# Kernel optimization log

Hardware: AMD Instinct MI355X
Metric: run time of the kernel (lower is better)

Reference implementation:

```python
import jax, jax.numpy as jnp
import numpy as np

B, C, H, W = 8, 512, 64, 64
S = 64
STD = 0.001  # torch init.normal_(weight, std=0.001)


def setup_inputs() -> dict:
    key = jax.random.key(0)
    ks = jax.random.split(key, 7)
    return {
        "queries": jax.random.normal(ks[0], (B, C, H, W), dtype=jnp.float32),
        "k": jax.random.normal(ks[1], (B, C, H, W), dtype=jnp.float32),
        "v": jax.random.normal(ks[2], (B, C, H, W), dtype=jnp.float32),
        "Wq": jax.random.normal(ks[3], (S, C), dtype=jnp.float32) * STD,
        "Wk": jax.random.normal(ks[4], (S, C), dtype=jnp.float32) * STD,
        "Wv": jax.random.normal(ks[5], (S, C), dtype=jnp.float32) * STD,
        "Wl": jax.random.normal(ks[6], (C, S), dtype=jnp.float32) * STD,
    }


def _branch(A, Bp, Cp, Wl):
    # A,Bp,Cp: [h,w,b,S] projected tensors
    m = jnp.einsum('hwbs,hwbt->hwst', A, Bp)          # [h,w,S,S]
    m = jax.nn.softmax(m, axis=1)                      # softmax over w (dim=1, as in torch)
    o = jnp.einsum('hwst,hwbt->hwsb', m, Cp)           # [h,w,S,b]
    o = o / jnp.sum(o, axis=2, keepdims=True)          # normalize over S
    o = jnp.einsum('hwsb,cs->hwbc', o, Wl)             # transpose + Linear(S->C)
    return jnp.transpose(o, (2, 3, 0, 1))              # [b,c,h,w]


def reference(queries, k, v, Wq, Wk, Wv, Wl):
    q = jnp.transpose(queries, (2, 3, 0, 1))  # [h,w,b,c]
    kk = jnp.transpose(k, (2, 3, 0, 1))
    vv = jnp.transpose(v, (2, 3, 0, 1))
    aq = jnp.einsum('hwbc,sc->hwbs', q, Wq)   # [h,w,b,S]
    ak = jnp.einsum('hwbc,sc->hwbs', kk, Wk)
    av = jnp.einsum('hwbc,sc->hwbs', vv, Wv)
    out_q = _branch(aq, ak, av, Wl)
    out_k = _branch(ak, av, aq, Wl)
    out_v = _branch(av, aq, ak, Wl)
    return jnp.concatenate((out_q, out_k, out_v), axis=0)  # [3b,c,h,w]
```

## Files before the change

### kernel.cpp

```cpp
#include <hip/hip_runtime.h>
#include <hip/hip_bf16.h>

#define HW 4096
#define CCH 512
#define SDIM 64
#define BDIM 8

typedef __attribute__((ext_vector_type(8))) short short8;
typedef __attribute__((ext_vector_type(4))) float f32x4;

static __device__ __forceinline__ ushort f2bf(float f) {
  __hip_bfloat16 h = __float2bfloat16(f);
  return *reinterpret_cast<ushort*>(&h);
}
static __device__ __forceinline__ float bf2f(ushort u) {
  union { unsigned int u32; float f; } c;
  c.u32 = ((unsigned int)u) << 16;
  return c.f;
}
static __device__ __forceinline__ ushort trunc_bf(float f, float* rem) {
  union { float f; unsigned int u; } a; a.f = f;
  union { float f; unsigned int u; } h; h.u = a.u & 0xFFFF0000u;
  *rem = f - h.f;
  return (ushort)(a.u >> 16);
}
static __device__ __forceinline__ ushort rne_bf(float f) {
  union { float f; unsigned int u; } a; a.f = f;
  return (ushort)((a.u + 0x8000u) >> 16);
}
static __device__ __forceinline__ void gll16(const float* g, float* lds_base) {
  __builtin_amdgcn_global_load_lds(
      (const __attribute__((address_space(1))) unsigned int*)g,
      (__attribute__((address_space(3))) unsigned int*)lds_base, 16, 0, 0);
}

__global__ __launch_bounds__(256) void prep_kernel(const float* __restrict__ Wq,
                                                   const float* __restrict__ Wk,
                                                   const float* __restrict__ Wv,
                                                   const float* __restrict__ Wl,
                                                   ushort* __restrict__ whi,
                                                   ushort* __restrict__ wmid,
                                                   ushort* __restrict__ wlo,
                                                   ushort* __restrict__ wlhi,
                                                   ushort* __restrict__ wllo) {
  const int idx = blockIdx.x * 1024 + threadIdx.x * 4;
  if (blockIdx.y == 3) {
    float4 f = *reinterpret_cast<const float4*>(&Wl[idx]);
    ushort4 h, l;
    float r;
    h.x = trunc_bf(f.x, &r); l.x = rne_bf(r);
    h.y = trunc_bf(f.y, &r); l.y = rne_bf(r);
    h.z = trunc_bf(f.z, &r); l.z = rne_bf(r);
    h.w = trunc_bf(f.w, &r); l.w = rne_bf(r);
    *reinterpret_cast<ushort4*>(&wlhi[idx]) = h;
    *reinterpret_cast<ushort4*>(&wllo[idx]) = l;
    return;
  }
  const float* W = blockIdx.y == 0 ? Wq : (blockIdx.y == 1 ? Wk : Wv);
  float4 f = *reinterpret_cast<const float4*>(&W[idx]);
  ushort4 h, m, l;
  float r, r2;
  h.x = f2bf(f.x); r = f.x - bf2f(h.x); m.x = f2bf(r); r2 = r - bf2f(m.x); l.x = f2bf(r2);
  h.y = f2bf(f.y); r = f.y - bf2f(h.y); m.y = f2bf(r); r2 = r - bf2f(m.y); l.y = f2bf(r2);
  h.z = f2bf(f.z); r = f.z - bf2f(h.z); m.z = f2bf(r); r2 = r - bf2f(m.z); l.z = f2bf(r2);
  h.w = f2bf(f.w); r = f.w - bf2f(h.w); m.w = f2bf(r); r2 = r - bf2f(m.w); l.w = f2bf(r2);
  const size_t o = (size_t)blockIdx.y * (SDIM * CCH) + idx;
  *reinterpret_cast<ushort4*>(&whi[o])  = h;
  *reinterpret_cast<ushort4*>(&wmid[o]) = m;
  *reinterpret_cast<ushort4*>(&wlo[o])  = l;
}

__global__ __launch_bounds__(256) void proj_mfma_kernel(const float* __restrict__ q,
                                                        const float* __restrict__ k,
                                                        const float* __restrict__ v,
                                                        const ushort* __restrict__ whi,
                                                        const ushort* __restrict__ wmid,
                                                        const ushort* __restrict__ wlo,
                                                        float* __restrict__ ap) {
  __shared__ float Xs[2 * 32 * 128];
  const int mt = blockIdx.x;
  const int b = blockIdx.y;
  const int br = blockIdx.z;
  const float* x = br == 0 ? q : (br == 1 ? k : v);
  const ushort* wh = whi + (size_t)br * SDIM * CCH;
  const ushort* wm = wmid + (size_t)br * SDIM * CCH;
  const ushort* wl = wlo + (size_t)br * SDIM * CCH;
  float* apo = ap + (size_t)br * HW * 512;
  const int hw0 = mt * 128;
  const int tid = threadIdx.x;
  const int l = tid & 63;
  const int wid = tid >> 6;
  const int wstrip = wid * 32;
  const int row16 = l & 15;
  const int kgrp = l >> 4;
  const float* xcol = x + (size_t)b * CCH * HW + hw0;
  const int rbase = 8 * wid;
  const int rsub = l >> 5;
  const int hws = (l & 31) * 4;

  f32x4 acc_hi[2][4] = {};
  f32x4 acc_co[2][4] = {};

#pragma unroll
  for (int j = 0; j < 4; ++j) {
    const int r = rbase + 2 * j + rsub;
    gll16(xcol + (size_t)r * HW + hws, &Xs[(rbase + 2 * j) * 128]);
  }

  for (int ci = 0; ci < 16; ++ci) {
    short8 bh[4], bm[4], bl[4];
#pragma unroll
    for (int nf = 0; nf < 4; ++nf) {
      const size_t off = (size_t)(nf * 16 + row16) * CCH + ci * 32 + kgrp * 8;
      bh[nf] = *reinterpret_cast<const short8*>(&wh[off]);
      bm[nf] = *reinterpret_cast<const short8*>(&wm[off]);
      bl[nf] = *reinterpret_cast<const short8*>(&wl[off]);
    }
    __builtin_amdgcn_sched_barrier(0);
    if (ci < 15) {
      float* dst = &Xs[((ci + 1) & 1) * 4096];
#pragma unroll
      for (int j = 0; j < 4; ++j) {
        const int r = rbase + 2 * j + rsub;
        gll16(xcol + (size_t)((ci + 1) * 32 + r) * HW + hws, dst + (rbase + 2 * j) * 128);
      }
      __builtin_amdgcn_sched_barrier(0);
      asm volatile("s_waitcnt vmcnt(4)" ::: "memory");
    } else {
      asm volatile("s_waitcnt vmcnt(0)" ::: "memory");
    }
    __builtin_amdgcn_sched_barrier(0);
    __builtin_amdgcn_s_barrier();
    __builtin_amdgcn_sched_barrier(0);

    const float* lw = &Xs[(ci & 1) * 4096];
#pragma unroll
    for (int mf = 0; mf < 2; ++mf) {
      const int rowA = wstrip + mf * 16 + row16;
      short8 ah, am, al;
      {
        ushort th[8], tm[8], tl[8];
#pragma unroll
        for (int i = 0; i < 8; ++i) {
          const float f = lw[(kgrp * 8 + i) * 128 + rowA];
          float r, r2;
          th[i] = trunc_bf(f, &r);
          tm[i] = trunc_bf(r, &r2);
          tl[i] = rne_bf(r2);
        }
        ah = *reinterpret_cast<const short8*>(th);
        am = *reinterpret_cast<const short8*>(tm);
        al = *reinterpret_cast<const short8*>(tl);
      }
#pragma unroll
      for (int nf = 0; nf < 4; ++nf) {
        acc_hi[mf][nf] = __builtin_amdgcn_mfma_f32_16x16x32_bf16(ah, bh[nf], acc_hi[mf][nf], 0, 0, 0);
        acc_co[mf][nf] = __builtin_amdgcn_mfma_f32_16x16x32_bf16(ah, bm[nf], acc_co[mf][nf], 0, 0, 0);
        acc_co[mf][nf] = __builtin_amdgcn_mfma_f32_16x16x32_bf16(am, bh[nf], acc_co[mf][nf], 0, 0, 0);
        acc_co[mf][nf] = __builtin_amdgcn_mfma_f32_16x16x32_bf16(am, bm[nf], acc_co[mf][nf], 0, 0, 0);
        acc_co[mf][nf] = __builtin_amdgcn_mfma_f32_16x16x32_bf16(ah, bl[nf], acc_co[mf][nf], 0, 0, 0);
        acc_co[mf][nf] = __builtin_amdgcn_mfma_f32_16x16x32_bf16(al, bh[nf], acc_co[mf][nf], 0, 0, 0);
        acc_co[mf][nf] = __builtin_amdgcn_mfma_f32_16x16x32_bf16(am, bl[nf], acc_co[mf][nf], 0, 0, 0);
        acc_co[mf][nf] = __builtin_amdgcn_mfma_f32_16x16x32_bf16(al, bm[nf], acc_co[mf][nf], 0, 0, 0);
      }
    }
    __builtin_amdgcn_sched_barrier(0);
    __builtin_amdgcn_s_barrier();
    __builtin_amdgcn_sched_barrier(0);
  }

#pragma unroll
  for (int mf = 0; mf < 2; ++mf)
#pragma unroll
    for (int nf = 0; nf < 4; ++nf)
#pragma unroll
      for (int r = 0; r < 4; ++r) {
        const int m = hw0 + wstrip + mf * 16 + kgrp * 4 + r;
        apo[(size_t)m * 512 + b * 64 + nf * 16 + row16] = acc_hi[mf][nf][r] + acc_co[mf][nf][r];
      }
}

__global__ __launch_bounds__(512) void denom_kernel(const float* __restrict__ ap,
                                                    float* __restrict__ rD) {
  __shared__ float As[8 * 16];
  __shared__ float Bs[8 * 64];
  const int h = blockIdx.x, br = blockIdx.y, sq = blockIdx.z;
  const float* A  = ap + ((size_t)br * HW + (size_t)h * 64) * (BDIM * SDIM);
  const float* Bp = ap + ((size_t)((br + 1) % 3) * HW + (size_t)h * 64) * (BDIM * SDIM);
  const int tid = threadIdx.x;
  const int t = tid & 63;
  const int sg = tid >> 6;
  float D[2] = {};
  for (int w = 0; w < 64; ++w) {
    __syncthreads();
    if (tid < 128) As[tid] = A[w * 512 + (tid >> 4) * 64 + sq * 16 + (tid & 15)];
    Bs[tid] = Bp[w * 512 + tid];
    __syncthreads();
    float bv[8];
#pragma unroll
    for (int b = 0; b < 8; ++b) bv[b] = Bs[b * 64 + t];
#pragma unroll
    for (int j = 0; j < 2; ++j) {
      const int sl = sg * 2 + j;
      float m = 0.f;
#pragma unroll
      for (int b = 0; b < 8; ++b) m = fmaf(As[b * 16 + sl], bv[b], m);
      D[j] += __expf(m);
    }
  }
#pragma unroll
  for (int j = 0; j < 2; ++j)
    rD[((size_t)(br * 64 + h) * 64 + sq * 16 + sg * 2 + j) * 64 + t] = 1.0f / D[j];
}

__global__ __launch_bounds__(256) void attn_kernel(const float* __restrict__ ap,
                                                   const float* __restrict__ rD,
                                                   float* __restrict__ on) {
  __shared__ float As[8 * 64], Bs[8 * 64], Cs[8 * 64];
  __shared__ float Ms[64 * 65];
  const int wc = blockIdx.x, h = blockIdx.y, br = blockIdx.z;
  const float* A  = ap + ((size_t)br * HW + h * 64) * 512;
  const float* Bp = ap + ((size_t)((br + 1) % 3) * HW + h * 64) * 512;
  const float* Cp = ap + ((size_t)((br + 2) % 3) * HW + h * 64) * 512;
  const float* rDp = rD + (size_t)(br * 64 + h) * 4096;
  const int tid = threadIdx.x;
  for (int w = wc * 8; w < wc * 8 + 8; ++w) {
    __syncthreads();
#pragma unroll
    for (int it = 0; it < 2; ++it) {
      int idx = it * 256 + tid;
      As[idx] = A[w * 512 + idx];
      Bs[idx] = Bp[w * 512 + idx];
      Cs[idx] = Cp[w * 512 + idx];
    }
    __syncthreads();
    {
      const int t = tid & 63, sg = tid >> 6;
      float bv[8];
#pragma unroll
      for (int b = 0; b < 8; ++b) bv[b] = Bs[b * 64 + t];
#pragma unroll
      for (int j = 0; j < 16; ++j) {
        int s = sg * 16 + j;
        float m = 0.f;
#pragma unroll
        for (int b = 0; b < 8; ++b) m = fmaf(As[b * 64 + s], bv[b], m);
        Ms[t * 65 + s] = __expf(m) * rDp[s * 64 + t];
      }
    }
    __syncthreads();
    const int s2 = tid & 63, bq = tid >> 6;
    float o0 = 0.f, o1 = 0.f;
#pragma unroll
    for (int tt = 0; tt < 64; tt += 4) {
      const float m0 = Ms[(tt + 0) * 65 + s2];
      const float m1 = Ms[(tt + 1) * 65 + s2];
      const float m2 = Ms[(tt + 2) * 65 + s2];
      const float m3 = Ms[(tt + 3) * 65 + s2];
      float4 c0 = *reinterpret_cast<const float4*>(&Cs[bq * 64 + tt]);
      float4 c1 = *reinterpret_cast<const float4*>(&Cs[(bq + 4) * 64 + tt]);
      o0 = fmaf(m3, c0.w, fmaf(m2, c0.z, fmaf(m1, c0.y, fmaf(m0, c0.x, o0))));
      o1 = fmaf(m3, c1.w, fmaf(m2, c1.z, fmaf(m1, c1.y, fmaf(m0, c1.x, o1))));
    }
    float n0 = o0, n1 = o1;
#pragma unroll
    for (int off = 32; off > 0; off >>= 1) {
      n0 += __shfl_xor(n0, off);
      n1 += __shfl_xor(n1, off);
    }
    const float r0 = 1.0f / n0, r1 = 1.0f / n1;
    const size_t ob = ((size_t)br * HW + h * 64 + w) * 512;
    on[ob + (size_t)bq * 64 + s2] = o0 * r0;
    on[ob + (size_t)(bq + 4) * 64 + s2] = o1 * r1;
  }
}

__global__ __launch_bounds__(256) void out_kernel(const float* __restrict__ on,
                                                  const ushort* __restrict__ wlhi,
                                                  const ushort* __restrict__ wllo,
                                                  float* __restrict__ out) {
  __shared__ float Os[128 * 68];
  const int hwt = blockIdx.x;
  const int brb = blockIdx.y;
  const int br = brb >> 3, b = brb & 7;
  const int hw0 = hwt * 128;
  const int tid = threadIdx.x;
  const int l = tid & 63;
  const int wv = tid >> 6;
  const int l15 = l & 15;
  const int kgrp = l >> 4;

  {
    const int row = tid >> 4;
    const int s4 = (tid & 15) * 4;
#pragma unroll
    for (int it = 0; it < 8; ++it) {
      const int r = row + it * 16;
      *reinterpret_cast<float4*>(&Os[r * 68 + s4]) =
          *reinterpret_cast<const float4*>(&on[((size_t)(br * HW + hw0 + r) * 8 + b) * 64 + s4]);
    }
  }
  __syncthreads();

  short8 onh[2][2], onl[2][2];
#pragma unroll
  for (int nf = 0; nf < 2; ++nf)
#pragma unroll
    for (int ks = 0; ks < 2; ++ks) {
      const int row = wv * 32 + nf * 16 + l15;
      const float* p = &Os[row * 68 + ks * 32 + kgrp * 8];
      ushort th[8], tl[8];
#pragma unroll
      for (int i = 0; i < 8; ++i) {
        float r;
        th[i] = trunc_bf(p[i], &r);
        tl[i] = rne_bf(r);
      }
      onh[nf][ks] = *reinterpret_cast<const short8*>(th);
      onl[nf][ks] = *reinterpret_cast<const short8*>(tl);
    }

  for (int mf = 0; mf < 32; ++mf) {
    f32x4 acc[2] = {};
#pragma unroll
    for (int ks = 0; ks < 2; ++ks) {
      const size_t woff = (size_t)(mf * 16 + l15) * 64 + ks * 32 + kgrp * 8;
      const short8 wh8 = *reinterpret_cast<const short8*>(&wlhi[woff]);
      const short8 wl8 = *reinterpret_cast<const short8*>(&wllo[woff]);
#pragma unroll
      for (int nf = 0; nf < 2; ++nf) {
        acc[nf] = __builtin_amdgcn_mfma_f32_16x16x32_bf16(wh8, onh[nf][ks], acc[nf], 0, 0, 0);
        acc[nf] = __builtin_amdgcn_mfma_f32_16x16x32_bf16(wh8, onl[nf][ks], acc[nf], 0, 0, 0);
        acc[nf] = __builtin_amdgcn_mfma_f32_16x16x32_bf16(wl8, onh[nf][ks], acc[nf], 0, 0, 0);
      }
    }
#pragma unroll
    for (int nf = 0; nf < 2; ++nf)
#pragma unroll
      for (int r = 0; r < 4; ++r) {
        const int cc = mf * 16 + kgrp * 4 + r;
        out[(size_t)(brb * 512 + cc) * HW + hw0 + wv * 32 + nf * 16 + l15] = acc[nf][r];
      }
  }
}

extern "C" void kernel_launch(void* const* d_in, const int* in_sizes, int n_in,
                              void* d_out, int out_size, void* d_ws, size_t ws_size,
                              hipStream_t stream) {
  const float* q  = (const float*)d_in[0];
  const float* k  = (const float*)d_in[1];
  const float* v  = (const float*)d_in[2];
  const float* Wq = (const float*)d_in[3];
  const float* Wk = (const float*)d_in[4];
  const float* Wv = (const float*)d_in[5];
  const float* Wl = (const float*)d_in[6];
  float* out = (float*)d_out;

  float* ap = (float*)d_ws;
  float* rD = ap + (size_t)3 * HW * 512;
  float* on = rD + (size_t)3 * 64 * 64 * 64;
  ushort* whi  = (ushort*)rD;
  ushort* wmid = whi + (size_t)3 * SDIM * CCH;
  ushort* wlo  = wmid + (size_t)3 * SDIM * CCH;
  ushort* wlhi = (ushort*)(on + (size_t)3 * HW * 512);
  ushort* wllo = wlhi + (size_t)SDIM * CCH;

  prep_kernel<<<dim3(32, 4), 256, 0, stream>>>(Wq, Wk, Wv, Wl, whi, wmid, wlo, wlhi, wllo);
  proj_mfma_kernel<<<dim3(32, 8, 3), 256, 0, stream>>>(q, k, v, whi, wmid, wlo, ap);
  denom_kernel<<<dim3(64, 3, 4), 512, 0, stream>>>(ap, rD);
  attn_kernel<<<dim3(8, 64, 3), 256, 0, stream>>>(ap, rD, on);
  out_kernel<<<dim3(32, 24), 256, 0, stream>>>(on, wlhi, wllo, out);
}
```

Before: 280.6 us.

## Stage projection weight splits through LDS with async loads and swizzle layouts

```diff
diff --git a/kernel.cpp b/kernel.cpp
--- a/kernel.cpp
+++ b/kernel.cpp
@@ -28,7 +28,7 @@
   union { float f; unsigned int u; } a; a.f = f;
   return (ushort)((a.u + 0x8000u) >> 16);
 }
-static __device__ __forceinline__ void gll16(const float* g, float* lds_base) {
+static __device__ __forceinline__ void gll16(const void* g, void* lds_base) {
   __builtin_amdgcn_global_load_lds(
       (const __attribute__((address_space(1))) unsigned int*)g,
       (__attribute__((address_space(3))) unsigned int*)lds_base, 16, 0, 0);
@@ -77,14 +77,15 @@
                                                         const ushort* __restrict__ wmid,
                                                         const ushort* __restrict__ wlo,
                                                         float* __restrict__ ap) {
-  __shared__ float Xs[2 * 32 * 128];
+  __shared__ float Xs[2][32 * 128];
+  __shared__ ushort Ws[2][3][64 * 32];
   const int mt = blockIdx.x;
   const int b = blockIdx.y;
   const int br = blockIdx.z;
   const float* x = br == 0 ? q : (br == 1 ? k : v);
-  const ushort* wh = whi + (size_t)br * SDIM * CCH;
-  const ushort* wm = wmid + (size_t)br * SDIM * CCH;
-  const ushort* wl = wlo + (size_t)br * SDIM * CCH;
+  const ushort* wsrc[3] = {whi + (size_t)br * SDIM * CCH,
+                           wmid + (size_t)br * SDIM * CCH,
+                           wlo + (size_t)br * SDIM * CCH};
   float* apo = ap + (size_t)br * HW * 512;
   const int hw0 = mt * 128;
   const int tid = threadIdx.x;
@@ -96,36 +97,37 @@
   const float* xcol = x + (size_t)b * CCH * HW + hw0;
   const int rbase = 8 * wid;
   const int rsub = l >> 5;
-  const int hws = (l & 31) * 4;
+  const int wrow = wid * 16 + (l >> 2);
+  const int wblk = (l & 3) ^ ((l >> 3) & 3);
+  const int jp = kgrp ^ ((row16 >> 1) & 3);
+  const int xswz = (kgrp & 1) << 4;
 
   f32x4 acc_hi[2][4] = {};
   f32x4 acc_co[2][4] = {};
 
-#pragma unroll
-  for (int j = 0; j < 4; ++j) {
-    const int r = rbase + 2 * j + rsub;
-    gll16(xcol + (size_t)r * HW + hws, &Xs[(rbase + 2 * j) * 128]);
-  }
+#define STAGE(BUF, CI)                                                            \
+  do {                                                                            \
+                      \
+    _Pragma("unroll") for (int j = 0; j < 4; ++j) {                               \
+      const int r = rbase + 2 * j + rsub;                                         \
+      const int hwsrc = (((l & 31) ^ ((((r) >> 3) & 1) << 2)) * 4);               \
+      gll16(xcol + (size_t)((CI) * 32 + r) * HW + hwsrc,                          \
+            &Xs[BUF][(rbase + 2 * j) * 128]);                                     \
+    }                                                                             \
+                            \
+    _Pragma("unroll") for (int lv = 0; lv < 3; ++lv)                              \
+      gll16(wsrc[lv] + (size_t)wrow * CCH + (CI) * 32 + wblk * 8,                 \
+            &Ws[BUF][lv][wid * 512]);                                             \
+  } while (0)
+
+  STAGE(0, 0);
 
   for (int ci = 0; ci < 16; ++ci) {
-    short8 bh[4], bm[4], bl[4];
-#pragma unroll
-    for (int nf = 0; nf < 4; ++nf) {
-      const size_t off = (size_t)(nf * 16 + row16) * CCH + ci * 32 + kgrp * 8;
-      bh[nf] = *reinterpret_cast<const short8*>(&wh[off]);
-      bm[nf] = *reinterpret_cast<const short8*>(&wm[off]);
-      bl[nf] = *reinterpret_cast<const short8*>(&wl[off]);
-    }
     __builtin_amdgcn_sched_barrier(0);
     if (ci < 15) {
-      float* dst = &Xs[((ci + 1) & 1) * 4096];
-#pragma unroll
-      for (int j = 0; j < 4; ++j) {
-        const int r = rbase + 2 * j + rsub;
-        gll16(xcol + (size_t)((ci + 1) * 32 + r) * HW + hws, dst + (rbase + 2 * j) * 128);
-      }
+      STAGE((ci + 1) & 1, ci + 1);
       __builtin_amdgcn_sched_barrier(0);
-      asm volatile("s_waitcnt vmcnt(4)" ::: "memory");
+      asm volatile("s_waitcnt vmcnt(7)" ::: "memory");
     } else {
       asm volatile("s_waitcnt vmcnt(0)" ::: "memory");
     }
@@ -133,10 +135,19 @@
     __builtin_amdgcn_s_barrier();
     __builtin_amdgcn_sched_barrier(0);
 
-    const float* lw = &Xs[(ci & 1) * 4096];
+    short8 bh[4], bm[4], bl[4];
+#pragma unroll
+    for (int nf = 0; nf < 4; ++nf) {
+      const int woff = (nf * 16 + row16) * 32 + jp * 8;
+      bh[nf] = *reinterpret_cast<const short8*>(&Ws[ci & 1][0][woff]);
+      bm[nf] = *reinterpret_cast<const short8*>(&Ws[ci & 1][1][woff]);
+      bl[nf] = *reinterpret_cast<const short8*>(&Ws[ci & 1][2][woff]);
+    }
+
+    const float* lw = &Xs[ci & 1][0];
 #pragma unroll
     for (int mf = 0; mf < 2; ++mf) {
-      const int rowA = wstrip + mf * 16 + row16;
+      const int rowA = (wstrip + mf * 16 + row16) ^ xswz;
       short8 ah, am, al;
       {
         ushort th[8], tm[8], tl[8];
@@ -168,6 +179,7 @@
     __builtin_amdgcn_s_barrier();
     __builtin_amdgcn_sched_barrier(0);
   }
+#undef STAGE
 
 #pragma unroll
   for (int mf = 0; mf < 2; ++mf)
```

After: 250.8 us. 1.12x faster.
